# Kernel optimization log

Hardware: AMD Instinct MI355X
Metric: run time of the kernel (lower is better)

The kernel has to match this reference:

```python
import jax, jax.numpy as jnp
import numpy as np

# ---- static config (matches init_kwargs) ----
N_LEVELS = 16
N_FEATS = 2
LOG2_HASHMAP_SIZE = 19
BASE_RES = 16.0
FINEST_RES = 512.0
N_POINTS = 1048576

_b = np.exp((np.log(FINEST_RES) - np.log(BASE_RES)) / (N_LEVELS - 1))
RESOLUTIONS = jnp.asarray(np.floor(BASE_RES * _b ** np.arange(N_LEVELS)), dtype=jnp.float32)  # [L]
BOX_MIN = jnp.array([-1.0, -1.0, -1.0], dtype=jnp.float32)
BOX_MAX = jnp.array([1.0, 1.0, 1.0], dtype=jnp.float32)
# corner offsets, ordering (i,j,k) with i outermost -> matches torch interpolation indexing
BOX_OFFSETS = jnp.array([[i, j, k] for i in (0, 1) for j in (0, 1) for k in (0, 1)], dtype=jnp.int32)  # [8,3]
PRIMES = jnp.array([1, 2654435761, 805459861], dtype=jnp.uint32)
HASH_MASK = jnp.uint32((1 << LOG2_HASHMAP_SIZE) - 1)


def _hash(coords):
    # coords: int32 [..., 3]; spatial hash with uint32 wrap-around multiply + xor
    c = coords.astype(jnp.uint32) * PRIMES
    h = c[..., 0] ^ c[..., 1] ^ c[..., 2]
    return (h & HASH_MASK).astype(jnp.int32)


def _level_embed(x, table, resolution):
    # x: [N,3] points, table: [T,F], resolution: scalar
    grid = (BOX_MAX - BOX_MIN) / resolution                      # [3]
    bl = jnp.floor((x - BOX_MIN) / grid).astype(jnp.int32)       # bottom-left voxel idx [N,3]
    vmin = bl.astype(x.dtype) * grid + BOX_MIN                   # [N,3]
    vmax = vmin + grid                                           # [N,3]
    idx = _hash(bl[:, None, :] + BOX_OFFSETS)                    # [N,8]
    voxels = table[idx]                                          # gather -> [N,8,F]
    w = (x - vmin) / (vmax - vmin)                               # [N,3]
    wx, wy, wz = w[:, 0:1], w[:, 1:2], w[:, 2:3]
    c00 = voxels[:, 0] * (1 - wx) + voxels[:, 4] * wx
    c01 = voxels[:, 1] * (1 - wx) + voxels[:, 5] * wx
    c10 = voxels[:, 2] * (1 - wx) + voxels[:, 6] * wx
    c11 = voxels[:, 3] * (1 - wx) + voxels[:, 7] * wx
    c0 = c00 * (1 - wy) + c10 * wy
    c1 = c01 * (1 - wy) + c11 * wy
    return c0 * (1 - wz) + c1 * wz                               # [N,F]


def setup_inputs() -> dict:
    key = jax.random.key(0)
    kx, kt = jax.random.split(key)
    x = jax.random.uniform(kx, (N_POINTS, 3), dtype=jnp.float32)  # points in [0,1)^3, inside box
    tables = jax.random.uniform(kt, (N_LEVELS, 1 << LOG2_HASHMAP_SIZE, N_FEATS),
                                dtype=jnp.float32, minval=-1e-4, maxval=1e-4)
    return {"x": x, "tables": tables}


def reference(x, tables):
    # vmap over the 16 hash-grid levels; each level hashes, gathers 8 corners, trilerps
    emb = jax.vmap(lambda t, r: _level_embed(x, t, r))(tables, RESOLUTIONS)  # [L,N,F]
    return jnp.transpose(emb, (1, 0, 2)).reshape(x.shape[0], N_LEVELS * N_FEATS)  # [N, L*F]
```

## Files before the change

### kernel.cpp

```cpp
#include <hip/hip_runtime.h>


#define TSIZE (1u << 19)
#define HMASK (TSIZE - 1u)
#define P1 2654435761u
#define P2 805459861u

typedef float f32x4 __attribute__((ext_vector_type(4)));
typedef float f32x2 __attribute__((ext_vector_type(2)));

__constant__ float RES_C[16] = {16.f, 20.f, 25.f, 32.f, 40.f, 50.f, 64.f, 80.f,
                                101.f, 128.f, 161.f, 203.f, 256.f, 322.f, 406.f, 512.f};

__global__ __launch_bounds__(256) void gather_level_kernel(
    const float* __restrict__ x,
    const float* __restrict__ tables,
    f32x2* __restrict__ ws,
    int npoints, int levelShift)
{
    const int level = blockIdx.x >> levelShift;
    const int chunk = blockIdx.x & ((1 << levelShift) - 1);
    const float halfr = 0.5f * RES_C[level];

    const float2* __restrict__ tab = (const float2*)tables + (size_t)level * TSIZE;
    f32x2* __restrict__ wrow = ws + (size_t)level * npoints;

#pragma unroll
    for (int q = 0; q < 2; ++q) {
        const int p = chunk * 512 + q * 256 + threadIdx.x;
        if (p >= npoints) break;

        const float fx = (x[3 * p + 0] + 1.0f) * halfr;
        const float fy = (x[3 * p + 1] + 1.0f) * halfr;
        const float fz = (x[3 * p + 2] + 1.0f) * halfr;

        const float bx = floorf(fx);
        const float by = floorf(fy);
        const float bz = floorf(fz);

        const float wx = fx - bx;
        const float wy = fy - by;
        const float wz = fz - bz;

        const unsigned ix0 = (unsigned)(int)bx;
        const unsigned iy0 = (unsigned)(int)by * P1;
        const unsigned iz0 = (unsigned)(int)bz * P2;
        const unsigned ix1 = ix0 + 1u;
        const unsigned iy1 = iy0 + P1;
        const unsigned iz1 = iz0 + P2;

        const float2 v000 = tab[(ix0 ^ iy0 ^ iz0) & HMASK];
        const float2 v001 = tab[(ix0 ^ iy0 ^ iz1) & HMASK];
        const float2 v010 = tab[(ix0 ^ iy1 ^ iz0) & HMASK];
        const float2 v011 = tab[(ix0 ^ iy1 ^ iz1) & HMASK];
        const float2 v100 = tab[(ix1 ^ iy0 ^ iz0) & HMASK];
        const float2 v101 = tab[(ix1 ^ iy0 ^ iz1) & HMASK];
        const float2 v110 = tab[(ix1 ^ iy1 ^ iz0) & HMASK];
        const float2 v111 = tab[(ix1 ^ iy1 ^ iz1) & HMASK];

        const float c00a = v000.x + wx * (v100.x - v000.x);
        const float c00b = v000.y + wx * (v100.y - v000.y);
        const float c01a = v001.x + wx * (v101.x - v001.x);
        const float c01b = v001.y + wx * (v101.y - v001.y);
        const float c10a = v010.x + wx * (v110.x - v010.x);
        const float c10b = v010.y + wx * (v110.y - v010.y);
        const float c11a = v011.x + wx * (v111.x - v011.x);
        const float c11b = v011.y + wx * (v111.y - v011.y);

        const float c0a = c00a + wy * (c10a - c00a);
        const float c0b = c00b + wy * (c10b - c00b);
        const float c1a = c01a + wy * (c11a - c01a);
        const float c1b = c01b + wy * (c11b - c01b);

        f32x2 r = { c0a + wz * (c1a - c0a), c0b + wz * (c1b - c0b) };
        __builtin_nontemporal_store(r, wrow + p);
    }
}

__global__ __launch_bounds__(256) void transpose_kernel(
    const f32x2* __restrict__ ws,
    float* __restrict__ out,
    int npoints)
{
    const int p = blockIdx.x * 256 + threadIdx.x;
    if (p >= npoints) return;

    f32x2 v[16];
#pragma unroll
    for (int l = 0; l < 16; ++l)
        v[l] = __builtin_nontemporal_load(ws + (size_t)l * npoints + p);

    f32x4* orow = (f32x4*)(out + (size_t)p * 32);
#pragma unroll
    for (int i = 0; i < 8; ++i) {
        f32x4 q = { v[2 * i].x, v[2 * i].y, v[2 * i + 1].x, v[2 * i + 1].y };
        orow[i] = q;
    }
}

__global__ __launch_bounds__(256) void hashgrid_fallback_kernel(
    const float* __restrict__ x,
    const float* __restrict__ tables,
    float* __restrict__ out)
{
    const int p = blockIdx.x * 256 + threadIdx.x;

    const float px = x[3 * p + 0] + 1.0f;
    const float py = x[3 * p + 1] + 1.0f;
    const float pz = x[3 * p + 2] + 1.0f;

    float acc[32];
    const float2* __restrict__ tab = (const float2*)tables;

#pragma unroll
    for (int l = 0; l < 16; ++l) {
        const float halfr = 0.5f * RES_C[l];
        const float fx = px * halfr, fy = py * halfr, fz = pz * halfr;
        const float bx = floorf(fx), by = floorf(fy), bz = floorf(fz);
        const float wx = fx - bx, wy = fy - by, wz = fz - bz;

        const unsigned ix0 = (unsigned)(int)bx;
        const unsigned iy0 = (unsigned)(int)by * P1;
        const unsigned iz0 = (unsigned)(int)bz * P2;
        const unsigned ix1 = ix0 + 1u, iy1 = iy0 + P1, iz1 = iz0 + P2;
        const unsigned base = (unsigned)l * TSIZE;

        const float2 v000 = tab[base + ((ix0 ^ iy0 ^ iz0) & HMASK)];
        const float2 v001 = tab[base + ((ix0 ^ iy0 ^ iz1) & HMASK)];
        const float2 v010 = tab[base + ((ix0 ^ iy1 ^ iz0) & HMASK)];
        const float2 v011 = tab[base + ((ix0 ^ iy1 ^ iz1) & HMASK)];
        const float2 v100 = tab[base + ((ix1 ^ iy0 ^ iz0) & HMASK)];
        const float2 v101 = tab[base + ((ix1 ^ iy0 ^ iz1) & HMASK)];
        const float2 v110 = tab[base + ((ix1 ^ iy1 ^ iz0) & HMASK)];
        const float2 v111 = tab[base + ((ix1 ^ iy1 ^ iz1) & HMASK)];

        const float c00a = v000.x + wx * (v100.x - v000.x);
        const float c00b = v000.y + wx * (v100.y - v000.y);
        const float c01a = v001.x + wx * (v101.x - v001.x);
        const float c01b = v001.y + wx * (v101.y - v001.y);
        const float c10a = v010.x + wx * (v110.x - v010.x);
        const float c10b = v010.y + wx * (v110.y - v010.y);
        const float c11a = v011.x + wx * (v111.x - v011.x);
        const float c11b = v011.y + wx * (v111.y - v011.y);

        const float c0a = c00a + wy * (c10a - c00a);
        const float c0b = c00b + wy * (c10b - c00b);
        const float c1a = c01a + wy * (c11a - c01a);
        const float c1b = c01b + wy * (c11b - c01b);

        acc[2 * l + 0] = c0a + wz * (c1a - c0a);
        acc[2 * l + 1] = c0b + wz * (c1b - c0b);
    }

    f32x4* orow = (f32x4*)(out + (size_t)p * 32);
#pragma unroll
    for (int i = 0; i < 8; ++i) {
        f32x4 v = { acc[4 * i + 0], acc[4 * i + 1], acc[4 * i + 2], acc[4 * i + 3] };
        orow[i] = v;
    }
}

extern "C" void kernel_launch(void* const* d_in, const int* in_sizes, int n_in,
                              void* d_out, int out_size, void* d_ws, size_t ws_size,
                              hipStream_t stream) {
    const float* x      = (const float*)d_in[0];
    const float* tables = (const float*)d_in[1];
    float* out          = (float*)d_out;

    const int npoints = in_sizes[0] / 3;
    const size_t ws_needed = (size_t)16 * npoints * sizeof(float2);

    if (ws_size >= ws_needed) {
        int chunks = (npoints + 511) / 512;
        int levelShift = 0;
        while ((1 << levelShift) < chunks) ++levelShift;

        dim3 blockA(256);
        dim3 gridA(16 << levelShift);
        hipLaunchKernelGGL(gather_level_kernel, gridA, blockA, 0, stream,
                           x, tables, (f32x2*)d_ws, npoints, levelShift);

        dim3 blockB(256);
        dim3 gridB((npoints + 255) / 256);
        hipLaunchKernelGGL(transpose_kernel, gridB, blockB, 0, stream,
                           (const f32x2*)d_ws, out, npoints);
    } else {
        dim3 block(256);
        dim3 grid((npoints + 255) / 256);
        hipLaunchKernelGGL(hashgrid_fallback_kernel, grid, block, 0, stream,
                           x, tables, out);
    }
}
```

Measured before the change: 569.3 us.

## Fuse gather and transpose into two level-half passes with LDS-staged stores

Replaces the per-level gather kernel plus separate transpose kernel with two launches, each handling 8 levels for 512 points per block. Results are staged through a padded shared-memory tile so each block writes coalesced 16-float halves of the output rows directly. This removes the workspace round trip (a 128 MB write and read) at the cost of each pass gathering from 8 hash tables at once, which enlarges the cache working set, and of two passes each writing half-rows.

Measured after the change: 605.7 us. 1.06x slower.

```diff
diff --git a/kernel.cpp b/kernel.cpp
--- a/kernel.cpp
+++ b/kernel.cpp
@@ -9,154 +9,143 @@
 typedef float f32x4 __attribute__((ext_vector_type(4)));
 typedef float f32x2 __attribute__((ext_vector_type(2)));
 
-__constant__ float RES_C[16] = {16.f, 20.f, 25.f, 32.f, 40.f, 50.f, 64.f, 80.f,
-                                101.f, 128.f, 161.f, 203.f, 256.f, 322.f, 406.f, 512.f};
+static constexpr float RES_K[16] = {16.f, 20.f, 25.f, 32.f, 40.f, 50.f, 64.f, 80.f,
+                                    101.f, 128.f, 161.f, 203.f, 256.f, 322.f, 406.f, 512.f};
 
-__global__ __launch_bounds__(256) void gather_level_kernel(
+__device__ __forceinline__ void gather_lerp(const float2* __restrict__ tab,
+                                            const float fx, const float fy, const float fz,
+                                            float& ra, float& rb)
+{
+    const float bx = floorf(fx), by = floorf(fy), bz = floorf(fz);
+    const float wx = fx - bx, wy = fy - by, wz = fz - bz;
+
+    const unsigned ix0 = (unsigned)(int)bx;
+    const unsigned iy0 = (unsigned)(int)by * P1;
+    const unsigned iz0 = (unsigned)(int)bz * P2;
+    const unsigned ix1 = ix0 + 1u, iy1 = iy0 + P1, iz1 = iz0 + P2;
+
+    const float2 v000 = tab[(ix0 ^ iy0 ^ iz0) & HMASK];
+    const float2 v001 = tab[(ix0 ^ iy0 ^ iz1) & HMASK];
+    const float2 v010 = tab[(ix0 ^ iy1 ^ iz0) & HMASK];
+    const float2 v011 = tab[(ix0 ^ iy1 ^ iz1) & HMASK];
+    const float2 v100 = tab[(ix1 ^ iy0 ^ iz0) & HMASK];
+    const float2 v101 = tab[(ix1 ^ iy0 ^ iz1) & HMASK];
+    const float2 v110 = tab[(ix1 ^ iy1 ^ iz0) & HMASK];
+    const float2 v111 = tab[(ix1 ^ iy1 ^ iz1) & HMASK];
+
+    const float c00a = v000.x + wx * (v100.x - v000.x);
+    const float c00b = v000.y + wx * (v100.y - v000.y);
+    const float c01a = v001.x + wx * (v101.x - v001.x);
+    const float c01b = v001.y + wx * (v101.y - v001.y);
+    const float c10a = v010.x + wx * (v110.x - v010.x);
+    const float c10b = v010.y + wx * (v110.y - v010.y);
+    const float c11a = v011.x + wx * (v111.x - v011.x);
+    const float c11b = v011.y + wx * (v111.y - v011.y);
+
+    const float c0a = c00a + wy * (c10a - c00a);
+    const float c0b = c00b + wy * (c10b - c00b);
+    const float c1a = c01a + wy * (c11a - c01a);
+    const float c1b = c01b + wy * (c11b - c01b);
+
+    ra = c0a + wz * (c1a - c0a);
+    rb = c0b + wz * (c1b - c0b);
+}
+
+template<int LBASE>
+__global__ __launch_bounds__(256) void fused_pass_kernel(
     const float* __restrict__ x,
     const float* __restrict__ tables,
-    f32x2* __restrict__ ws,
-    int npoints, int levelShift)
-{
-    const int level = blockIdx.x >> levelShift;
-    const int chunk = blockIdx.x & ((1 << levelShift) - 1);
-    const float halfr = 0.5f * RES_C[level];
-
-    const float2* __restrict__ tab = (const float2*)tables + (size_t)level * TSIZE;
-    f32x2* __restrict__ wrow = ws + (size_t)level * npoints;
-
-#pragma unroll
-    for (int q = 0; q < 2; ++q) {
-        const int p = chunk * 512 + q * 256 + threadIdx.x;
-        if (p >= npoints) break;
-
-        const float fx = (x[3 * p + 0] + 1.0f) * halfr;
-        const float fy = (x[3 * p + 1] + 1.0f) * halfr;
-        const float fz = (x[3 * p + 2] + 1.0f) * halfr;
-
-        const float bx = floorf(fx);
-        const float by = floorf(fy);
-        const float bz = floorf(fz);
-
-        const float wx = fx - bx;
-        const float wy = fy - by;
-        const float wz = fz - bz;
-
-        const unsigned ix0 = (unsigned)(int)bx;
-        const unsigned iy0 = (unsigned)(int)by * P1;
-        const unsigned iz0 = (unsigned)(int)bz * P2;
-        const unsigned ix1 = ix0 + 1u;
-        const unsigned iy1 = iy0 + P1;
-        const unsigned iz1 = iz0 + P2;
-
-        const float2 v000 = tab[(ix0 ^ iy0 ^ iz0) & HMASK];
-        const float2 v001 = tab[(ix0 ^ iy0 ^ iz1) & HMASK];
-        const float2 v010 = tab[(ix0 ^ iy1 ^ iz0) & HMASK];
-        const float2 v011 = tab[(ix0 ^ iy1 ^ iz1) & HMASK];
-        const float2 v100 = tab[(ix1 ^ iy0 ^ iz0) & HMASK];
-        const float2 v101 = tab[(ix1 ^ iy0 ^ iz1) & HMASK];
-        const float2 v110 = tab[(ix1 ^ iy1 ^ iz0) & HMASK];
-        const float2 v111 = tab[(ix1 ^ iy1 ^ iz1) & HMASK];
-
-        const float c00a = v000.x + wx * (v100.x - v000.x);
-        const float c00b = v000.y + wx * (v100.y - v000.y);
-        const float c01a = v001.x + wx * (v101.x - v001.x);
-        const float c01b = v001.y + wx * (v101.y - v001.y);
-        const float c10a = v010.x + wx * (v110.x - v010.x);
-        const float c10b = v010.y + wx * (v110.y - v010.y);
-        const float c11a = v011.x + wx * (v111.x - v011.x);
-        const float c11b = v011.y + wx * (v111.y - v011.y);
-
-        const float c0a = c00a + wy * (c10a - c00a);
-        const float c0b = c00b + wy * (c10b - c00b);
-        const float c1a = c01a + wy * (c11a - c01a);
-        const float c1b = c01b + wy * (c11b - c01b);
-
-        f32x2 r = { c0a + wz * (c1a - c0a), c0b + wz * (c1b - c0b) };
-        __builtin_nontemporal_store(r, wrow + p);
-    }
-}
-
-__global__ __launch_bounds__(256) void transpose_kernel(
-    const f32x2* __restrict__ ws,
     float* __restrict__ out,
     int npoints)
 {
-    const int p = blockIdx.x * 256 + threadIdx.x;
-    if (p >= npoints) return;
+    __shared__ float tile[256 * 17];
 
-    f32x2 v[16];
-#pragma unroll
-    for (int l = 0; l < 16; ++l)
-        v[l] = __builtin_nontemporal_load(ws + (size_t)l * npoints + p);
+    const int t  = threadIdx.x;
+    const int P0 = blockIdx.x * 512;
+    constexpr int PASSF = (LBASE / 8) * 16;
 
-    f32x4* orow = (f32x4*)(out + (size_t)p * 32);
-#pragma unroll
-    for (int i = 0; i < 8; ++i) {
-        f32x4 q = { v[2 * i].x, v[2 * i].y, v[2 * i + 1].x, v[2 * i + 1].y };
-        orow[i] = q;
-    }
-}
+    if (P0 + 512 <= npoints) {
+        const int pA = P0 + t;
+        const int pB = P0 + 256 + t;
 
-__global__ __launch_bounds__(256) void hashgrid_fallback_kernel(
-    const float* __restrict__ x,
-    const float* __restrict__ tables,
-    float* __restrict__ out)
-{
-    const int p = blockIdx.x * 256 + threadIdx.x;
+        const float ax = x[3 * pA + 0] + 1.0f;
+        const float ay = x[3 * pA + 1] + 1.0f;
+        const float az = x[3 * pA + 2] + 1.0f;
+        const float bx = x[3 * pB + 0] + 1.0f;
+        const float by = x[3 * pB + 1] + 1.0f;
+        const float bz = x[3 * pB + 2] + 1.0f;
 
-    const float px = x[3 * p + 0] + 1.0f;
-    const float py = x[3 * p + 1] + 1.0f;
-    const float pz = x[3 * p + 2] + 1.0f;
-
-    float acc[32];
-    const float2* __restrict__ tab = (const float2*)tables;
+        float acc[32];
 
 #pragma unroll
-    for (int l = 0; l < 16; ++l) {
-        const float halfr = 0.5f * RES_C[l];
-        const float fx = px * halfr, fy = py * halfr, fz = pz * halfr;
-        const float bx = floorf(fx), by = floorf(fy), bz = floorf(fz);
-        const float wx = fx - bx, wy = fy - by, wz = fz - bz;
+        for (int l = 0; l < 8; ++l) {
+            const float halfr = 0.5f * RES_K[LBASE + l];
+            const float2* __restrict__ tab =
+                (const float2*)tables + (size_t)(LBASE + l) * TSIZE;
+            gather_lerp(tab, ax * halfr, ay * halfr, az * halfr,
+                        acc[2 * l], acc[2 * l + 1]);
+            gather_lerp(tab, bx * halfr, by * halfr, bz * halfr,
+                        acc[16 + 2 * l], acc[16 + 2 * l + 1]);
+        }
 
-        const unsigned ix0 = (unsigned)(int)bx;
-        const unsigned iy0 = (unsigned)(int)by * P1;
-        const unsigned iz0 = (unsigned)(int)bz * P2;
-        const unsigned ix1 = ix0 + 1u, iy1 = iy0 + P1, iz1 = iz0 + P2;
-        const unsigned base = (unsigned)l * TSIZE;
+#pragma unroll
+        for (int i = 0; i < 16; ++i)
+            tile[t * 17 + i] = acc[i];
+        __syncthreads();
+        {
+            float* obase = out + (size_t)P0 * 32 + PASSF;
+#pragma unroll
+            for (int k = 0; k < 4; ++k) {
+                const int s  = k * 256 + t;
+                const int pt = s >> 2;
+                const int c  = s & 3;
+                f32x4 q = { tile[pt * 17 + 4 * c + 0], tile[pt * 17 + 4 * c + 1],
+                            tile[pt * 17 + 4 * c + 2], tile[pt * 17 + 4 * c + 3] };
+                __builtin_nontemporal_store(q, (f32x4*)(obase + (size_t)pt * 32 + 4 * c));
+            }
+        }
+        __syncthreads();
 
-        const float2 v000 = tab[base + ((ix0 ^ iy0 ^ iz0) & HMASK)];
-        const float2 v001 = tab[base + ((ix0 ^ iy0 ^ iz1) & HMASK)];
-        const float2 v010 = tab[base + ((ix0 ^ iy1 ^ iz0) & HMASK)];
-        const float2 v011 = tab[base + ((ix0 ^ iy1 ^ iz1) & HMASK)];
-        const float2 v100 = tab[base + ((ix1 ^ iy0 ^ iz0) & HMASK)];
-        const float2 v101 = tab[base + ((ix1 ^ iy0 ^ iz1) & HMASK)];
-        const float2 v110 = tab[base + ((ix1 ^ iy1 ^ iz0) & HMASK)];
-        const float2 v111 = tab[base + ((ix1 ^ iy1 ^ iz1) & HMASK)];
-
-        const float c00a = v000.x + wx * (v100.x - v000.x);
-        const float c00b = v000.y + wx * (v100.y - v000.y);
-        const float c01a = v001.x + wx * (v101.x - v001.x);
-        const float c01b = v001.y + wx * (v101.y - v001.y);
-        const float c10a = v010.x + wx * (v110.x - v010.x);
-        const float c10b = v010.y + wx * (v110.y - v010.y);
-        const float c11a = v011.x + wx * (v111.x - v011.x);
-        const float c11b = v011.y + wx * (v111.y - v011.y);
-
-        const float c0a = c00a + wy * (c10a - c00a);
-        const float c0b = c00b + wy * (c10b - c00b);
-        const float c1a = c01a + wy * (c11a - c01a);
-        const float c1b = c01b + wy * (c11b - c01b);
-
-        acc[2 * l + 0] = c0a + wz * (c1a - c0a);
-        acc[2 * l + 1] = c0b + wz * (c1b - c0b);
-    }
-
-    f32x4* orow = (f32x4*)(out + (size_t)p * 32);
 #pragma unroll
-    for (int i = 0; i < 8; ++i) {
-        f32x4 v = { acc[4 * i + 0], acc[4 * i + 1], acc[4 * i + 2], acc[4 * i + 3] };
-        orow[i] = v;
+        for (int i = 0; i < 16; ++i)
+            tile[t * 17 + i] = acc[16 + i];
+        __syncthreads();
+        {
+            float* obase = out + (size_t)(P0 + 256) * 32 + PASSF;
+#pragma unroll
+            for (int k = 0; k < 4; ++k) {
+                const int s  = k * 256 + t;
+                const int pt = s >> 2;
+                const int c  = s & 3;
+                f32x4 q = { tile[pt * 17 + 4 * c + 0], tile[pt * 17 + 4 * c + 1],
+                            tile[pt * 17 + 4 * c + 2], tile[pt * 17 + 4 * c + 3] };
+                __builtin_nontemporal_store(q, (f32x4*)(obase + (size_t)pt * 32 + 4 * c));
+            }
+        }
+    } else {
+#pragma unroll
+        for (int q = 0; q < 2; ++q) {
+            const int p = P0 + q * 256 + t;
+            if (p >= npoints) continue;
+            const float px = x[3 * p + 0] + 1.0f;
+            const float py = x[3 * p + 1] + 1.0f;
+            const float pz = x[3 * p + 2] + 1.0f;
+            float r[16];
+#pragma unroll
+            for (int l = 0; l < 8; ++l) {
+                const float halfr = 0.5f * RES_K[LBASE + l];
+                const float2* __restrict__ tab =
+                    (const float2*)tables + (size_t)(LBASE + l) * TSIZE;
+                gather_lerp(tab, px * halfr, py * halfr, pz * halfr,
+                            r[2 * l], r[2 * l + 1]);
+            }
+            float* orow = out + (size_t)p * 32 + PASSF;
+#pragma unroll
+            for (int i = 0; i < 4; ++i) {
+                f32x4 v = { r[4 * i + 0], r[4 * i + 1], r[4 * i + 2], r[4 * i + 3] };
+                *(f32x4*)(orow + 4 * i) = v;
+            }
+        }
     }
 }
 
@@ -168,26 +157,12 @@
     float* out          = (float*)d_out;
 
     const int npoints = in_sizes[0] / 3;
-    const size_t ws_needed = (size_t)16 * npoints * sizeof(float2);
 
-    if (ws_size >= ws_needed) {
-        int chunks = (npoints + 511) / 512;
-        int levelShift = 0;
-        while ((1 << levelShift) < chunks) ++levelShift;
+    dim3 block(256);
+    dim3 grid((npoints + 511) / 512);
 
-        dim3 blockA(256);
-        dim3 gridA(16 << levelShift);
-        hipLaunchKernelGGL(gather_level_kernel, gridA, blockA, 0, stream,
-                           x, tables, (f32x2*)d_ws, npoints, levelShift);
-
-        dim3 blockB(256);
-        dim3 gridB((npoints + 255) / 256);
-        hipLaunchKernelGGL(transpose_kernel, gridB, blockB, 0, stream,
-                           (const f32x2*)d_ws, out, npoints);
-    } else {
-        dim3 block(256);
-        dim3 grid((npoints + 255) / 256);
-        hipLaunchKernelGGL(hashgrid_fallback_kernel, grid, block, 0, stream,
-                           x, tables, out);
-    }
+    hipLaunchKernelGGL(fused_pass_kernel<0>, grid, block, 0, stream,
+                       x, tables, out, npoints);
+    hipLaunchKernelGGL(fused_pass_kernel<8>, grid, block, 0, stream,
+                       x, tables, out, npoints);
 }
```
